# Kernel tuning notes

Hardware: AMD Instinct MI355X
Metric: run time of the kernel (lower is better)

Reference implementation:

```python
import jax, jax.numpy as jnp
import numpy as np

B, T, E, H = 256, 256, 384, 64  # batch, seq (== block_size), embed_dim, head_size

def setup_inputs() -> dict:
    key = jax.random.key(0)
    kx, kq, kk, kv = jax.random.split(key, 4)
    scale = 1.0 / np.sqrt(E)
    return {
        "x": jax.random.normal(kx, (B, T, E), dtype=jnp.float32),
        "Wq": jax.random.normal(kq, (E, H), dtype=jnp.float32) * scale,
        "Wk": jax.random.normal(kk, (E, H), dtype=jnp.float32) * scale,
        "Wv": jax.random.normal(kv, (E, H), dtype=jnp.float32) * scale,
    }

def reference(x, Wq, Wk, Wv):
    # Linear projections (bias-free), faithful to nn.Linear(embed_dim, head_size, bias=False)
    q = jnp.einsum("bte,eh->bth", x, Wq)
    k = jnp.einsum("bte,eh->bth", x, Wk)
    v = jnp.einsum("bte,eh->bth", x, Wv)
    # Scaled QK^T with causal mask, softmax, weighted sum.
    # Dropout is identity in eval mode (reference is deterministic).
    wei = jnp.einsum("bth,bsh->bts", q, k) * (H ** -0.5)  # [B, T, T]
    causal = jnp.tril(jnp.ones((T, T), dtype=bool))
    wei = jnp.where(causal, wei, -jnp.inf)
    wei = jax.nn.softmax(wei, axis=-1)
    out = jnp.einsum("bts,bsh->bth", wei, v)  # [B, T, H]
    return out
```

## Files before the change

### kernel.cpp

```cpp
#include <hip/hip_runtime.h>
#include <hip/hip_bf16.h>

typedef __attribute__((ext_vector_type(8))) short short8;
typedef __attribute__((ext_vector_type(4))) float f32x4;

#define MFMA(a, b, c) __builtin_amdgcn_mfma_f32_16x16x32_bf16((a), (b), (c), 0, 0, 0)

__device__ __forceinline__ unsigned short f2bf(float f) {
  union { float f; unsigned int u; } v; v.f = f;
  unsigned int u = v.u;
  unsigned int r = u + 0x7FFFu + ((u >> 16) & 1u);
  return (unsigned short)(r >> 16);
}

__device__ __forceinline__ unsigned int f2bf2(float a, float b) {
  __hip_bfloat162 h2 = __float22bfloat162_rn(make_float2(a, b));
  union { __hip_bfloat162 h; unsigned int u; } cv; cv.h = h2;
  return cv.u;
}

__global__ void wconv_kernel(const float* __restrict__ Wq, const float* __restrict__ Wk,
                             const float* __restrict__ Wv, unsigned short* __restrict__ W3t) {
  int n = blockIdx.x;
  int k = threadIdx.x;
  const float* src = (n < 64) ? Wq : ((n < 128) ? Wk : Wv);
  W3t[n * 384 + k] = f2bf(src[k * 64 + (n & 63)]);
}

__global__ __launch_bounds__(1024) void fused_kernel(
    const float* __restrict__ x, const unsigned short* __restrict__ W3t,
    float* __restrict__ out) {
  extern __shared__ unsigned short sm[];
  unsigned short* Ql = sm;
  unsigned short* Kl = sm + 18432;
  unsigned short* Vl = sm + 36864;

  const int tid = threadIdx.x;
  const int w = tid >> 6, lane = tid & 63, g = lane >> 4, q = lane & 15;
  const int b = blockIdx.x;
  const float* xb = x + (long)b * 256 * 384;

  f32x4 acc[12];
  const f32x4 zf = {0.f, 0.f, 0.f, 0.f};
#pragma unroll
  for (int j = 0; j < 12; ++j) acc[j] = zf;

  float4 xr0, xr1;
  uint4 wr1;
  const bool wact = (tid < 768);
  const int wn = tid >> 2, wk = (tid & 3) * 8;
  const int xrow0 = tid >> 3, xrow1 = (tid + 1024) >> 3, xc4 = (tid & 7) * 4;

  auto LOAD = [&](int k0) {
    xr0 = *(const float4*)&xb[xrow0 * 384 + k0 + xc4];
    xr1 = *(const float4*)&xb[xrow1 * 384 + k0 + xc4];
    if (wact) wr1 = *(const uint4*)&W3t[wn * 384 + k0 + wk];
  };
  auto WRITE = [&](int bufofs) {
    uint2 p0, p1;
    p0.x = f2bf2(xr0.x, xr0.y); p0.y = f2bf2(xr0.z, xr0.w);
    p1.x = f2bf2(xr1.x, xr1.y); p1.y = f2bf2(xr1.z, xr1.w);
    *(uint2*)&sm[bufofs + xrow0 * 40 + xc4] = p0;
    *(uint2*)&sm[bufofs + xrow1 * 40 + xc4] = p1;
    if (wact) *(uint4*)&sm[bufofs + 10240 + wn * 40 + wk] = wr1;
  };
  auto STEP = [&](int bufofs) {
    const unsigned short* xlb = sm + bufofs;
    const unsigned short* wlb = sm + bufofs + 10240;
    short8 a0 = *(const short8*)&xlb[(16 * w + q) * 40 + g * 8];
#pragma unroll
    for (int ct = 0; ct < 12; ++ct) {
      short8 bfr = *(const short8*)&wlb[(16 * ct + q) * 40 + g * 8];
      acc[ct] = MFMA(a0, bfr, acc[ct]);
    }
  };

  LOAD(0);
#pragma unroll
  for (int s = 0; s < 12; ++s) {
    const int bo = (s & 1) ? 17920 : 0;
    WRITE(bo);
    if (s < 11) LOAD(32 * (s + 1));
    __syncthreads();
    STEP(bo);
  }
  __syncthreads();

  {
    const int mb = 16 * w + 4 * g;
#pragma unroll
    for (int ct = 0; ct < 12; ++ct) {
      int c = 16 * ct + q;
      unsigned int p01 = f2bf2(acc[ct][0], acc[ct][1]);
      unsigned int p23 = f2bf2(acc[ct][2], acc[ct][3]);
      unsigned short h0 = (unsigned short)p01, h1 = (unsigned short)(p01 >> 16);
      unsigned short h2 = (unsigned short)p23, h3 = (unsigned short)(p23 >> 16);
      if (ct < 4) {
        Ql[(mb + 0) * 72 + c] = h0; Ql[(mb + 1) * 72 + c] = h1;
        Ql[(mb + 2) * 72 + c] = h2; Ql[(mb + 3) * 72 + c] = h3;
      } else if (ct < 8) {
        int cc = c - 64;
        Kl[(mb + 0) * 72 + cc] = h0; Kl[(mb + 1) * 72 + cc] = h1;
        Kl[(mb + 2) * 72 + cc] = h2; Kl[(mb + 3) * 72 + cc] = h3;
      } else {
        int hh = c - 128;
        uint2 pk; pk.x = p01; pk.y = p23;
        *(uint2*)&Vl[hh * 264 + mb] = pk;
      }
    }
  }
  __syncthreads();

  unsigned short* Pb = sm + 53760 + w * 640;
  const float SCL = 0.125f * 1.4426950408889634f;
  const int t = w;

  short8 aq0 = *(const short8*)&Ql[(16 * t + q) * 72 + g * 8];
  short8 aq1 = *(const short8*)&Ql[(16 * t + q) * 72 + 32 + g * 8];

  f32x4 o[4];
#pragma unroll
  for (int ct = 0; ct < 4; ++ct) o[ct] = zf;
  float mrow[4] = {-1e30f, -1e30f, -1e30f, -1e30f};
  float lrow[4] = {0.f, 0.f, 0.f, 0.f};

#pragma unroll
  for (int ks = 0; ks < 8; ++ks) {
    if (2 * ks <= t) {
      const int j0 = 2 * ks, j1 = 2 * ks + 1;
      const bool has1 = (j1 <= t);
      short8 bk0a = *(const short8*)&Kl[(16 * j0 + q) * 72 + g * 8];
      short8 bk0b = *(const short8*)&Kl[(16 * j0 + q) * 72 + 32 + g * 8];
      f32x4 s0 = MFMA(aq0, bk0a, zf);
      s0 = MFMA(aq1, bk0b, s0);
      f32x4 s1;
      if (has1) {
        short8 bk1a = *(const short8*)&Kl[(16 * j1 + q) * 72 + g * 8];
        short8 bk1b = *(const short8*)&Kl[(16 * j1 + q) * 72 + 32 + g * 8];
        s1 = MFMA(aq0, bk1a, zf);
        s1 = MFMA(aq1, bk1b, s1);
      }
      float p0[4], p1[4];
#pragma unroll
      for (int jr = 0; jr < 4; ++jr) {
        float v0 = s0[jr] * SCL;
        if (j0 == t && q > 4 * g + jr) v0 = -1e30f;
        float v1 = -1e30f;
        if (has1) {
          v1 = s1[jr] * SCL;
          if (j1 == t && q > 4 * g + jr) v1 = -1e30f;
        }
        float loc = fmaxf(v0, v1);
        loc = fmaxf(loc, __shfl_xor(loc, 1));
        loc = fmaxf(loc, __shfl_xor(loc, 2));
        loc = fmaxf(loc, __shfl_xor(loc, 4));
        loc = fmaxf(loc, __shfl_xor(loc, 8));
        float mnew = fmaxf(mrow[jr], loc);
        float f = exp2f(mrow[jr] - mnew);
        mrow[jr] = mnew;
        p0[jr] = exp2f(v0 - mnew);
        p1[jr] = exp2f(v1 - mnew);
        lrow[jr] = lrow[jr] * f + p0[jr] + p1[jr];
        o[0][jr] *= f; o[1][jr] *= f; o[2][jr] *= f; o[3][jr] *= f;
      }
      unsigned int a01 = f2bf2(p0[0], p0[1]), a23 = f2bf2(p0[2], p0[3]);
      unsigned int b01 = f2bf2(p1[0], p1[1]), b23 = f2bf2(p1[2], p1[3]);
      Pb[(4 * g + 0) * 40 + q]      = (unsigned short)a01;
      Pb[(4 * g + 1) * 40 + q]      = (unsigned short)(a01 >> 16);
      Pb[(4 * g + 2) * 40 + q]      = (unsigned short)a23;
      Pb[(4 * g + 3) * 40 + q]      = (unsigned short)(a23 >> 16);
      Pb[(4 * g + 0) * 40 + 16 + q] = (unsigned short)b01;
      Pb[(4 * g + 1) * 40 + 16 + q] = (unsigned short)(b01 >> 16);
      Pb[(4 * g + 2) * 40 + 16 + q] = (unsigned short)b23;
      Pb[(4 * g + 3) * 40 + 16 + q] = (unsigned short)(b23 >> 16);
      short8 ap = *(const short8*)&Pb[q * 40 + g * 8];
#pragma unroll
      for (int ct = 0; ct < 4; ++ct) {
        short8 bv = *(const short8*)&Vl[(16 * ct + q) * 264 + ks * 32 + g * 8];
        o[ct] = MFMA(ap, bv, o[ct]);
      }
    }
  }

  const long rowbase = (long)b * 256 + 16 * t + 4 * g;
#pragma unroll
  for (int jr = 0; jr < 4; ++jr) {
    float l = lrow[jr];
    l += __shfl_xor(l, 1);
    l += __shfl_xor(l, 2);
    l += __shfl_xor(l, 4);
    l += __shfl_xor(l, 8);
    float inv = 1.0f / l;
#pragma unroll
    for (int ct = 0; ct < 4; ++ct) {
      out[(rowbase + jr) * 64 + 16 * ct + q] = o[ct][jr] * inv;
    }
  }
}

extern "C" void kernel_launch(void* const* d_in, const int* in_sizes, int n_in,
                              void* d_out, int out_size, void* d_ws, size_t ws_size,
                              hipStream_t stream) {
  const float* x  = (const float*)d_in[0];
  const float* Wq = (const float*)d_in[1];
  const float* Wk = (const float*)d_in[2];
  const float* Wv = (const float*)d_in[3];
  float* out = (float*)d_out;

  unsigned short* W3t = (unsigned short*)d_ws;

  hipFuncSetAttribute((const void*)fused_kernel,
                      hipFuncAttributeMaxDynamicSharedMemorySize, 128000);

  wconv_kernel<<<192, 384, 0, stream>>>(Wq, Wk, Wv, W3t);
  fused_kernel<<<256, 1024, 128000, stream>>>(x, W3t, out);
}
```

Measured before the change: 40.15 us.

## Pre-swizzle weights into MFMA fragment layout, load x directly, transpose score MFMA

The weight conversion kernel now writes bf16 weights in per-lane MFMA fragment order, so the fused kernel can copy all of W into LDS once and read fragments contiguously. x rows are loaded straight from global memory into registers and converted, which removes the per-step LDS staging and barriers of the double-buffered projection loop. The attention loop computes S transposed (K as the A operand), so row max and sum reduce across lane groups with two shuffles instead of four. It also writes P with vectorized stores and uses a runtime trip count instead of masked unrolled iterations. The cost is a larger LDS allocation (147456 bytes) and uncoalesced per-lane x loads from global memory.

```diff
diff --git a/kernel.cpp b/kernel.cpp
--- a/kernel.cpp
+++ b/kernel.cpp
@@ -5,13 +5,6 @@
 typedef __attribute__((ext_vector_type(4))) float f32x4;
 
 #define MFMA(a, b, c) __builtin_amdgcn_mfma_f32_16x16x32_bf16((a), (b), (c), 0, 0, 0)
-
-__device__ __forceinline__ unsigned short f2bf(float f) {
-  union { float f; unsigned int u; } v; v.f = f;
-  unsigned int u = v.u;
-  unsigned int r = u + 0x7FFFu + ((u >> 16) & 1u);
-  return (unsigned short)(r >> 16);
-}
 
 __device__ __forceinline__ unsigned int f2bf2(float a, float b) {
   __hip_bfloat162 h2 = __float22bfloat162_rn(make_float2(a, b));
@@ -21,10 +14,20 @@
 
 __global__ void wconv_kernel(const float* __restrict__ Wq, const float* __restrict__ Wk,
                              const float* __restrict__ Wv, unsigned short* __restrict__ W3t) {
-  int n = blockIdx.x;
-  int k = threadIdx.x;
-  const float* src = (n < 64) ? Wq : ((n < 128) ? Wk : Wv);
-  W3t[n * 384 + k] = f2bf(src[k * 64 + (n & 63)]);
+  int j = blockIdx.x * 256 + threadIdx.x;
+  int s = j / 768;
+  int r = j - s * 768;
+  int ct = r >> 6, l = r & 63, g = l >> 4, q = l & 15;
+  const float* src = (ct < 4) ? Wq : ((ct < 8) ? Wk : Wv);
+  int col = 16 * (ct & 3) + q;
+  int k = 32 * s + 8 * g;
+  float e[8];
+#pragma unroll
+  for (int i = 0; i < 8; ++i) e[i] = src[(k + i) * 64 + col];
+  uint4 u;
+  u.x = f2bf2(e[0], e[1]); u.y = f2bf2(e[2], e[3]);
+  u.z = f2bf2(e[4], e[5]); u.w = f2bf2(e[6], e[7]);
+  *(uint4*)&W3t[j * 8] = u;
 }
 
 __global__ __launch_bounds__(1024) void fused_kernel(
@@ -38,51 +41,43 @@
   const int tid = threadIdx.x;
   const int w = tid >> 6, lane = tid & 63, g = lane >> 4, q = lane & 15;
   const int b = blockIdx.x;
-  const float* xb = x + (long)b * 256 * 384;
+  const float* xb = x + (long)b * 98304;
+
+#pragma unroll
+  for (int i = 0; i < 9; ++i) {
+    int idx = tid + i * 1024;
+    *(uint4*)&sm[idx * 8] = *(const uint4*)&W3t[idx * 8];
+  }
 
   f32x4 acc[12];
   const f32x4 zf = {0.f, 0.f, 0.f, 0.f};
 #pragma unroll
   for (int j = 0; j < 12; ++j) acc[j] = zf;
 
-  float4 xr0, xr1;
-  uint4 wr1;
-  const bool wact = (tid < 768);
-  const int wn = tid >> 2, wk = (tid & 3) * 8;
-  const int xrow0 = tid >> 3, xrow1 = (tid + 1024) >> 3, xc4 = (tid & 7) * 4;
-
-  auto LOAD = [&](int k0) {
-    xr0 = *(const float4*)&xb[xrow0 * 384 + k0 + xc4];
-    xr1 = *(const float4*)&xb[xrow1 * 384 + k0 + xc4];
-    if (wact) wr1 = *(const uint4*)&W3t[wn * 384 + k0 + wk];
-  };
-  auto WRITE = [&](int bufofs) {
-    uint2 p0, p1;
-    p0.x = f2bf2(xr0.x, xr0.y); p0.y = f2bf2(xr0.z, xr0.w);
-    p1.x = f2bf2(xr1.x, xr1.y); p1.y = f2bf2(xr1.z, xr1.w);
-    *(uint2*)&sm[bufofs + xrow0 * 40 + xc4] = p0;
-    *(uint2*)&sm[bufofs + xrow1 * 40 + xc4] = p1;
-    if (wact) *(uint4*)&sm[bufofs + 10240 + wn * 40 + wk] = wr1;
-  };
-  auto STEP = [&](int bufofs) {
-    const unsigned short* xlb = sm + bufofs;
-    const unsigned short* wlb = sm + bufofs + 10240;
-    short8 a0 = *(const short8*)&xlb[(16 * w + q) * 40 + g * 8];
+  const float* xrow = xb + (16 * w + q) * 384 + 8 * g;
+  float4 x0 = *(const float4*)&xrow[0];
+  float4 x1 = *(const float4*)&xrow[4];
+
+  __syncthreads();
+
+#pragma unroll
+  for (int ks = 0; ks < 12; ++ks) {
+    float4 n0, n1;
+    if (ks < 11) {
+      n0 = *(const float4*)&xrow[32 * (ks + 1)];
+      n1 = *(const float4*)&xrow[32 * (ks + 1) + 4];
+    }
+    uint4 au;
+    au.x = f2bf2(x0.x, x0.y); au.y = f2bf2(x0.z, x0.w);
+    au.z = f2bf2(x1.x, x1.y); au.w = f2bf2(x1.z, x1.w);
+    union { uint4 u; short8 s8; } av; av.u = au;
+    const unsigned short* wbase = sm + ks * 6144 + lane * 8;
 #pragma unroll
     for (int ct = 0; ct < 12; ++ct) {
-      short8 bfr = *(const short8*)&wlb[(16 * ct + q) * 40 + g * 8];
-      acc[ct] = MFMA(a0, bfr, acc[ct]);
-    }
-  };
-
-  LOAD(0);
-#pragma unroll
-  for (int s = 0; s < 12; ++s) {
-    const int bo = (s & 1) ? 17920 : 0;
-    WRITE(bo);
-    if (s < 11) LOAD(32 * (s + 1));
-    __syncthreads();
-    STEP(bo);
+      short8 bfr = *(const short8*)&wbase[ct * 512];
+      acc[ct] = MFMA(av.s8, bfr, acc[ct]);
+    }
+    if (ks < 11) { x0 = n0; x1 = n1; }
   }
   __syncthreads();
 
@@ -121,79 +116,75 @@
   f32x4 o[4];
 #pragma unroll
   for (int ct = 0; ct < 4; ++ct) o[ct] = zf;
-  float mrow[4] = {-1e30f, -1e30f, -1e30f, -1e30f};
-  float lrow[4] = {0.f, 0.f, 0.f, 0.f};
-
-#pragma unroll
-  for (int ks = 0; ks < 8; ++ks) {
-    if (2 * ks <= t) {
-      const int j0 = 2 * ks, j1 = 2 * ks + 1;
-      const bool has1 = (j1 <= t);
-      short8 bk0a = *(const short8*)&Kl[(16 * j0 + q) * 72 + g * 8];
-      short8 bk0b = *(const short8*)&Kl[(16 * j0 + q) * 72 + 32 + g * 8];
-      f32x4 s0 = MFMA(aq0, bk0a, zf);
-      s0 = MFMA(aq1, bk0b, s0);
-      f32x4 s1;
-      if (has1) {
-        short8 bk1a = *(const short8*)&Kl[(16 * j1 + q) * 72 + g * 8];
-        short8 bk1b = *(const short8*)&Kl[(16 * j1 + q) * 72 + 32 + g * 8];
-        s1 = MFMA(aq0, bk1a, zf);
-        s1 = MFMA(aq1, bk1b, s1);
-      }
-      float p0[4], p1[4];
-#pragma unroll
-      for (int jr = 0; jr < 4; ++jr) {
-        float v0 = s0[jr] * SCL;
-        if (j0 == t && q > 4 * g + jr) v0 = -1e30f;
-        float v1 = -1e30f;
-        if (has1) {
-          v1 = s1[jr] * SCL;
-          if (j1 == t && q > 4 * g + jr) v1 = -1e30f;
-        }
-        float loc = fmaxf(v0, v1);
-        loc = fmaxf(loc, __shfl_xor(loc, 1));
-        loc = fmaxf(loc, __shfl_xor(loc, 2));
-        loc = fmaxf(loc, __shfl_xor(loc, 4));
-        loc = fmaxf(loc, __shfl_xor(loc, 8));
-        float mnew = fmaxf(mrow[jr], loc);
-        float f = exp2f(mrow[jr] - mnew);
-        mrow[jr] = mnew;
-        p0[jr] = exp2f(v0 - mnew);
-        p1[jr] = exp2f(v1 - mnew);
-        lrow[jr] = lrow[jr] * f + p0[jr] + p1[jr];
-        o[0][jr] *= f; o[1][jr] *= f; o[2][jr] *= f; o[3][jr] *= f;
-      }
-      unsigned int a01 = f2bf2(p0[0], p0[1]), a23 = f2bf2(p0[2], p0[3]);
-      unsigned int b01 = f2bf2(p1[0], p1[1]), b23 = f2bf2(p1[2], p1[3]);
-      Pb[(4 * g + 0) * 40 + q]      = (unsigned short)a01;
-      Pb[(4 * g + 1) * 40 + q]      = (unsigned short)(a01 >> 16);
-      Pb[(4 * g + 2) * 40 + q]      = (unsigned short)a23;
-      Pb[(4 * g + 3) * 40 + q]      = (unsigned short)(a23 >> 16);
-      Pb[(4 * g + 0) * 40 + 16 + q] = (unsigned short)b01;
-      Pb[(4 * g + 1) * 40 + 16 + q] = (unsigned short)(b01 >> 16);
-      Pb[(4 * g + 2) * 40 + 16 + q] = (unsigned short)b23;
-      Pb[(4 * g + 3) * 40 + 16 + q] = (unsigned short)(b23 >> 16);
-      short8 ap = *(const short8*)&Pb[q * 40 + g * 8];
-#pragma unroll
-      for (int ct = 0; ct < 4; ++ct) {
-        short8 bv = *(const short8*)&Vl[(16 * ct + q) * 264 + ks * 32 + g * 8];
-        o[ct] = MFMA(ap, bv, o[ct]);
-      }
-    }
-  }
-
-  const long rowbase = (long)b * 256 + 16 * t + 4 * g;
+  float m = -1e30f;
+  float lsum = 0.f;
+
+  const int KS = (t >> 1) + 1;
+  for (int ks = 0; ks < KS; ++ks) {
+    const int j0 = 2 * ks, j1 = 2 * ks + 1;
+    const bool has1 = (j1 <= t);
+    short8 ka0 = *(const short8*)&Kl[(16 * j0 + q) * 72 + g * 8];
+    short8 ka1 = *(const short8*)&Kl[(16 * j0 + q) * 72 + 32 + g * 8];
+    f32x4 s0 = MFMA(ka0, aq0, zf);
+    s0 = MFMA(ka1, aq1, s0);
+    f32x4 s1 = zf;
+    if (has1) {
+      short8 kb0 = *(const short8*)&Kl[(16 * j1 + q) * 72 + g * 8];
+      short8 kb1 = *(const short8*)&Kl[(16 * j1 + q) * 72 + 32 + g * 8];
+      s1 = MFMA(kb0, aq0, zf);
+      s1 = MFMA(kb1, aq1, s1);
+    }
+    float v[8];
+#pragma unroll
+    for (int jr = 0; jr < 4; ++jr) {
+      float a = s0[jr] * SCL;
+      if (j0 == t && 4 * g + jr > q) a = -1e30f;
+      v[jr] = a;
+      float c = has1 ? s1[jr] * SCL : -1e30f;
+      if (has1 && j1 == t && 4 * g + jr > q) c = -1e30f;
+      v[4 + jr] = c;
+    }
+    float mloc = fmaxf(fmaxf(fmaxf(v[0], v[1]), fmaxf(v[2], v[3])),
+                       fmaxf(fmaxf(v[4], v[5]), fmaxf(v[6], v[7])));
+    mloc = fmaxf(mloc, __shfl_xor(mloc, 16));
+    mloc = fmaxf(mloc, __shfl_xor(mloc, 32));
+    float mnew = fmaxf(m, mloc);
+    float f = exp2f(m - mnew);
+    m = mnew;
+    float p[8];
+    float ls = 0.f;
+#pragma unroll
+    for (int i = 0; i < 8; ++i) { p[i] = exp2f(v[i] - mnew); ls += p[i]; }
+    lsum = lsum * f + ls;
+#pragma unroll
+    for (int jr = 0; jr < 4; ++jr) {
+      float fr = __shfl(f, 4 * g + jr);
+      o[0][jr] *= fr; o[1][jr] *= fr; o[2][jr] *= fr; o[3][jr] *= fr;
+    }
+    uint2 pa; pa.x = f2bf2(p[0], p[1]); pa.y = f2bf2(p[2], p[3]);
+    *(uint2*)&Pb[q * 40 + 4 * g] = pa;
+    uint2 pc; pc.x = f2bf2(p[4], p[5]); pc.y = f2bf2(p[6], p[7]);
+    *(uint2*)&Pb[q * 40 + 16 + 4 * g] = pc;
+    short8 ap = *(const short8*)&Pb[q * 40 + g * 8];
+#pragma unroll
+    for (int ct = 0; ct < 4; ++ct) {
+      short8 bv = *(const short8*)&Vl[(16 * ct + q) * 264 + ks * 32 + g * 8];
+      o[ct] = MFMA(ap, bv, o[ct]);
+    }
+  }
+
+  lsum += __shfl_xor(lsum, 16);
+  lsum += __shfl_xor(lsum, 32);
+  float linv[4];
+#pragma unroll
+  for (int jr = 0; jr < 4; ++jr) linv[jr] = 1.0f / __shfl(lsum, 4 * g + jr);
+
+  const long rowbase = (long)b * 256 + 16 * t;
 #pragma unroll
   for (int jr = 0; jr < 4; ++jr) {
-    float l = lrow[jr];
-    l += __shfl_xor(l, 1);
-    l += __shfl_xor(l, 2);
-    l += __shfl_xor(l, 4);
-    l += __shfl_xor(l, 8);
-    float inv = 1.0f / l;
 #pragma unroll
     for (int ct = 0; ct < 4; ++ct) {
-      out[(rowbase + jr) * 64 + 16 * ct + q] = o[ct][jr] * inv;
+      out[(rowbase + 4 * g + jr) * 64 + 16 * ct + q] = o[ct][jr] * linv[jr];
     }
   }
 }
@@ -210,8 +201,8 @@
   unsigned short* W3t = (unsigned short*)d_ws;
 
   hipFuncSetAttribute((const void*)fused_kernel,
-                      hipFuncAttributeMaxDynamicSharedMemorySize, 128000);
-
-  wconv_kernel<<<192, 384, 0, stream>>>(Wq, Wk, Wv, W3t);
-  fused_kernel<<<256, 1024, 128000, stream>>>(x, W3t, out);
-}
+                      hipFuncAttributeMaxDynamicSharedMemorySize, 147456);
+
+  wconv_kernel<<<36, 256, 0, stream>>>(Wq, Wk, Wv, W3t);
+  fused_kernel<<<256, 1024, 147456, stream>>>(x, W3t, out);
+}
```

Result: faster. 36.95 us (-8.0%).
